# Optimization experiments

Measured on AMD Instinct MI355X. Metric: run time of the kernel, lower is better.

Reference implementation:

```python
import jax, jax.numpy as jnp
import numpy as np

N_P, N_V, N_C, N_A = 8000, 3000, 1500, 6000
CLS = N_C
D = 128
E = 150000
N_TOT = N_P + N_V + N_C + N_A
LAMBDA1 = 1.0


def _cal_matrix(A):
    # row-normalize, leaving all-zero rows untouched (matches cal_matrix)
    d = jnp.sum(A, axis=1)
    safe = jnp.where(d > 0, d, 1.0)
    return jnp.where((d > 0)[:, None], A / safe[:, None], A)


def _linear(x, W, b):
    return x @ W.T + b


def _gru(x, h, Wih, Whh, bih, bhh):
    # torch.nn.GRUCell semantics; gate order r, z, n
    gi = x @ Wih.T + bih
    gh = h @ Whh.T + bhh
    ir, iz, inn = jnp.split(gi, 3, axis=1)
    hr, hz, hn = jnp.split(gh, 3, axis=1)
    r = jax.nn.sigmoid(ir + hr)
    z = jax.nn.sigmoid(iz + hz)
    n = jnp.tanh(inn + r * hn)
    return (1.0 - z) * n + z * h


def _ce_soft(pred, label):
    # torch CrossEntropyLoss with probabilistic targets; NOTE: pred is already
    # softmaxed in the original, so log_softmax is applied on top (faithful double softmax)
    return -jnp.mean(jnp.sum(label * jax.nn.log_softmax(pred, axis=1), axis=1))


def _fuse(e0, e1, W2, b2, W3, b3):
    # attention fusion: leaky_relu(., 0) == relu; softmax over the NODE axis (faithful)
    a = jnp.concatenate([_linear(e0, W2, b2), _linear(e1, W3, b3)], axis=0)  # [2N,1]
    alpha = jax.nn.softmax(jax.nn.relu(a).reshape(2, -1, 1), axis=1)
    return jax.nn.relu(jnp.sum(alpha * jnp.stack([e0, e1], axis=0), axis=0))


def _forward(feat_P, feat_V, feat_C, feat_A, W1, b1, W2, b2, W3, b3,
             L00W, L00b, L01W, L01b, L10W, L10b, L11W, L11b, L12W, L12b,
             g0_Wih, g0_Whh, g0_bih, g0_bhh, g1_Wih, g1_Whh, g1_bih, g1_bhh,
             rel_emb, adj00, adj01, adj10, adj11, adj12, clsA, clsP, clsV, u_s, u_d):
    # self embeddings via shared linear1
    self_P = _linear(feat_P, W1, b1)
    self_V = _linear(feat_V, W1, b1)
    self_C = _linear(feat_C, W1, b1)
    self_A = _linear(feat_A, W1, b1)
    loss_tcp = jnp.float32(0.0)
    # ---- meta-path 0: V -> P -> A (GRUCell 0) ----
    pred = jax.nn.softmax(_linear(feat_V, L00W, L00b), axis=1)        # [N_V, CLS]
    loss_tcp += _ce_soft(pred, clsV)
    tcp = jnp.sum(pred * clsV, axis=1, keepdims=True)                 # bmm([N,1,C],[N,C,1])
    h = adj00 @ (tcp * feat_V)                                        # [N_P, D]
    state_P0 = _gru(feat_P, h, g0_Wih, g0_Whh, g0_bih, g0_bhh)
    pred = jax.nn.softmax(_linear(state_P0, L01W, L01b), axis=1)
    loss_tcp += _ce_soft(pred, clsP)
    tcp = jnp.sum(pred * clsP, axis=1, keepdims=True)
    h = adj01 @ (tcp * state_P0)                                      # [N_A, D]
    state_A0 = _gru(feat_A, h, g0_Wih, g0_Whh, g0_bih, g0_bhh)
    # ---- meta-path 1: A -> P -> V -> C (GRUCell 1) ----
    pred = jax.nn.softmax(_linear(feat_A, L10W, L10b), axis=1)
    loss_tcp += _ce_soft(pred, clsA)
    tcp = jnp.sum(pred * clsA, axis=1, keepdims=True)
    h = adj10 @ (tcp * feat_A)                                        # [N_P, D]
    state_P1 = _gru(feat_P, h, g1_Wih, g1_Whh, g1_bih, g1_bhh)        # appended 3rd, unused by fusion
    pred = jax.nn.softmax(_linear(state_P1, L11W, L11b), axis=1)
    loss_tcp += _ce_soft(pred, clsP)
    tcp = jnp.sum(pred * clsP, axis=1, keepdims=True)
    h = adj11 @ (tcp * state_P1)                                      # [N_V, D]
    state_V1 = _gru(feat_V, h, g1_Wih, g1_Whh, g1_bih, g1_bhh)
    pred = jax.nn.softmax(_linear(state_V1, L12W, L12b), axis=1)
    loss_tcp += _ce_soft(pred, clsV)
    tcp = jnp.sum(pred * clsV, axis=1, keepdims=True)
    h = adj12 @ (tcp * state_V1)                                      # [N_C, D]
    state_C1 = _gru(feat_C, h, g1_Wih, g1_Whh, g1_bih, g1_bhh)
    # ---- attention fusion of (self_emb, first GRU state) per node type ----
    emb_P = _fuse(self_P, state_P0, W2, b2, W3, b3)
    emb_V = _fuse(self_V, state_V1, W2, b2, W3, b3)
    emb_C = _fuse(self_C, state_C1, W2, b2, W3, b3)
    emb_A = _fuse(self_A, state_A0, W2, b2, W3, b3)
    final_ent = jnp.concatenate([emb_P, emb_V, emb_C, emb_A], axis=0)  # order P,V,C,A
    # ---- link scoring ----
    lab_d = u_d[:, 2].astype(jnp.float32)
    lab_s = u_s[:, 2].astype(jnp.float32)
    M_r = rel_emb[u_d[:, 3]]
    inner_d = jnp.sum(M_r * jnp.tanh(final_ent[u_d[:, 0]] + final_ent[u_d[:, 1]]), axis=1)
    inner_s = jnp.sum(final_ent[u_s[:, 0]] * final_ent[u_s[:, 1]], axis=1)
    base = -jnp.sum(jax.nn.log_sigmoid(lab_d * inner_d)) - jnp.sum(jax.nn.log_sigmoid(lab_s * inner_s))
    # l2_loss_emb is 0 in the original; l2_loss is computed but never added to loss_emb
    loss = base + LAMBDA1 * loss_tcp
    return loss, final_ent, rel_emb


def setup_inputs():
    key = jax.random.key(0)
    ki = iter(jax.random.split(key, 48))
    def nk():
        return next(ki)
    def xav(o, i):  # xavier_normal_
        return jax.random.normal(nk(), (o, i), jnp.float32) * jnp.sqrt(2.0 / (o + i))
    def uni(shape):  # torch GRUCell default init
        k = 1.0 / float(np.sqrt(D))
        return jax.random.uniform(nk(), shape, jnp.float32, -k, k)
    def radj(o, i, p=0.003):  # raw binary adjacency
        return (jax.random.uniform(nk(), (o, i)) < p).astype(jnp.float32)

    feat_P = jax.random.normal(nk(), (N_P, D), jnp.float32)
    feat_V = jax.random.normal(nk(), (N_V, D), jnp.float32)
    feat_C = jax.random.normal(nk(), (N_C, D), jnp.float32)
    feat_A = jax.random.normal(nk(), (N_A, D), jnp.float32)
    A00 = radj(N_P, N_V); A01 = radj(N_A, N_P)
    A10 = radj(N_P, N_A); A11 = radj(N_V, N_P); A12 = radj(N_C, N_V)

    inp = dict(
        feat_P=feat_P, feat_V=feat_V, feat_C=feat_C, feat_A=feat_A,
        W1=xav(D, D), b1=jnp.zeros((D,), jnp.float32),
        W2=xav(1, D), b2=jnp.zeros((1,), jnp.float32),
        W3=xav(1, D), b3=jnp.zeros((1,), jnp.float32),
        L00W=xav(CLS, D), L00b=jnp.zeros((CLS,), jnp.float32),
        L01W=xav(CLS, D), L01b=jnp.zeros((CLS,), jnp.float32),
        L10W=xav(CLS, D), L10b=jnp.zeros((CLS,), jnp.float32),
        L11W=xav(CLS, D), L11b=jnp.zeros((CLS,), jnp.float32),
        L12W=xav(CLS, D), L12b=jnp.zeros((CLS,), jnp.float32),
        g0_Wih=uni((3 * D, D)), g0_Whh=uni((3 * D, D)), g0_bih=uni((3 * D,)), g0_bhh=uni((3 * D,)),
        g1_Wih=uni((3 * D, D)), g1_Whh=uni((3 * D, D)), g1_bih=uni((3 * D,)), g1_bhh=uni((3 * D,)),
        rel_emb=jax.random.normal(nk(), (12, D), jnp.float32),
        adj00=_cal_matrix(A00), adj01=_cal_matrix(A01),
        adj10=_cal_matrix(A10), adj11=_cal_matrix(A11), adj12=_cal_matrix(A12),
        clsA=_cal_matrix((A12 @ (A11 @ A10)).T),   # [N_A, CLS]
        clsP=_cal_matrix((A12 @ A11).T),           # [N_P, CLS]
        clsV=_cal_matrix(A12.T),                   # [N_V, CLS]
    )

    def edges(n_cols):
        i = jax.random.randint(nk(), (E,), 0, N_TOT)
        j = jax.random.randint(nk(), (E,), 0, N_TOT)
        lab = jax.random.randint(nk(), (E,), 0, 2) * 2 - 1  # labels in {-1,+1}
        cols = [i, j, lab]
        if n_cols == 4:
            cols.append(jax.random.randint(nk(), (E,), 0, 12))
        return jnp.stack(cols, axis=1)

    inp['u_s'] = edges(3)
    inp['u_d'] = edges(4)
    return inp


def reference(feat_P, feat_V, feat_C, feat_A, W1, b1, W2, b2, W3, b3,
              L00W, L00b, L01W, L01b, L10W, L10b, L11W, L11b, L12W, L12b,
              g0_Wih, g0_Whh, g0_bih, g0_bhh, g1_Wih, g1_Whh, g1_bih, g1_bhh,
              rel_emb, adj00, adj01, adj10, adj11, adj12, clsA, clsP, clsV, u_s, u_d):
    return _forward(feat_P, feat_V, feat_C, feat_A, W1, b1, W2, b2, W3, b3,
                    L00W, L00b, L01W, L01b, L10W, L10b, L11W, L11b, L12W, L12b,
                    g0_Wih, g0_Whh, g0_bih, g0_bhh, g1_Wih, g1_Whh, g1_bih, g1_bhh,
                    rel_emb, adj00, adj01, adj10, adj11, adj12, clsA, clsP, clsV, u_s, u_d)
```

## Files before the change

### kernel.cpp

```cpp
#include <hip/hip_runtime.h>
#include <cstdint>
#include <cstddef>

#define DEV_INLINE __device__ __forceinline__

typedef __attribute__((ext_vector_type(8))) short bf16x8;
typedef __attribute__((ext_vector_type(16))) float f32x16;
struct __align__(8) US4 { unsigned short u[4]; };

DEV_INLINE unsigned short f2bf(float x) {
  unsigned u = __float_as_uint(x);
  return (unsigned short)((u + 0x7FFFu + ((u >> 16) & 1u)) >> 16);
}
DEV_INLINE float2 bfpair(unsigned v) {
  return make_float2(__uint_as_float(v << 16), __uint_as_float(v & 0xFFFF0000u));
}

struct CvtSeg { const float* src; unsigned short* dst; int n; int nblk; };
struct CvtArgs { CvtSeg seg[16]; int nseg; };

__global__ __launch_bounds__(256) void convert_bf16_many(CvtArgs args) {
  int b = blockIdx.x;
  int s = 0;
  while (s < args.nseg && b >= args.seg[s].nblk) { b -= args.seg[s].nblk; ++s; }
// ... 51 lines not shown
    acc1 = __builtin_amdgcn_mfma_f32_32x32x16_bf16(a, b1, acc1, 0, 0, 0);
  }

#pragma unroll
  for (int reg = 0; reg < 16; ++reg) {
    int r = bm + wave * 32 + (reg & 3) + 8 * (reg >> 2) + 4 * lhi;
    if (r < N) {
      int c0 = bn + l31;
      if (c0 < O) C[(size_t)r * O + c0] = acc0[reg] + bias[c0];
      int c1 = bn + 32 + l31;
      if (c1 < O) C[(size_t)r * O + c1] = acc1[reg] + bias[c1];
    }
  }
}

__global__ __launch_bounds__(256) void gemm_bf16(
    const unsigned short* __restrict__ Xb, const unsigned short* __restrict__ Wb,
    const float* __restrict__ bias, float* __restrict__ C, int N, int O)
{
  __shared__ __align__(16) unsigned short Xs[128 * 128];
  __shared__ __align__(16) unsigned short Ws[64 * 128];
  gemm_body(Xb, Wb, bias, C, N, O, blockIdx.x * 128, blockIdx.y * 64, Xs, Ws);
}

struct GSeg { const unsigned short* X; const unsigned short* W; const float* bias;
              float* C; int N; int O; int blk0; int xblk; };
struct GSegs { GSeg s[8]; int nseg; };

__global__ __launch_bounds__(256) void gemm_bf16_gseg(GSegs gs) {
  __shared__ __align__(16) unsigned short Xs[128 * 128];
  __shared__ __align__(16) unsigned short Ws[64 * 128];
  int bx = blockIdx.x;
  int si = 0;
  while (si + 1 < gs.nseg && bx >= gs.s[si + 1].blk0) ++si;
  const GSeg& g = gs.s[si];
  int b = bx - g.blk0;
  int bm = (b % g.xblk) * 128;
  int bn = (b / g.xblk) * 64;
  gemm_body(g.X, g.W, g.bias, g.C, g.N, g.O, bm, bn, Xs, Ws);
}

DEV_INLINE void ghgru_body(
    const unsigned short* __restrict__ Hb, const unsigned short* __restrict__ Whhb,
    const float* __restrict__ bhh, const float* __restrict__ gi,
    const float* __restrict__ hv, float* __restrict__ out,
    unsigned short* __restrict__ outb, int M, int bm, unsigned short* As)
{
  const int tid = threadIdx.x;
#pragma unroll
  for (int i = 0; i < 2; ++i) {
    int s = tid + 256 * i;
    int row = s >> 4, c16 = s & 15;
    uint4 v = make_uint4(0, 0, 0, 0);
    int gr = bm + row;
    if (gr < M) v = *reinterpret_cast<const uint4*>(Hb + (size_t)gr * 128 + c16 * 8);
    *reinterpret_cast<uint4*>(&As[(row * 16 + (c16 ^ (row & 7))) * 8]) = v;
  }
  __syncthreads();

  const int wave = tid >> 6, lane = tid & 63;
  const int l31 = lane & 31, lhi = lane >> 5;
  const int d = wave * 32 + l31;

  f32x16 ar, az, an;
#pragma unroll
  for (int i = 0; i < 16; ++i) { ar[i] = 0.f; az[i] = 0.f; an[i] = 0.f; }

#pragma unroll
  for (int ks = 0; ks < 8; ++ks) {
    int c16 = ks * 2 + lhi;
    bf16x8 a = *reinterpret_cast<const bf16x8*>(&As[(l31 * 16 + (c16 ^ (l31 & 7))) * 8]);
    const unsigned short* wb = Whhb + (size_t)c16 * 8;
    bf16x8 br = *reinterpret_cast<const bf16x8*>(wb + (size_t)d * 128);
    bf16x8 bz = *reinterpret_cast<const bf16x8*>(wb + (size_t)(128 + d) * 128);
    bf16x8 bn = *reinterpret_cast<const bf16x8*>(wb + (size_t)(256 + d) * 128);
    ar = __builtin_amdgcn_mfma_f32_32x32x16_bf16(a, br, ar, 0, 0, 0);
    az = __builtin_amdgcn_mfma_f32_32x32x16_bf16(a, bz, az, 0, 0, 0);
    an = __builtin_amdgcn_mfma_f32_32x32x16_bf16(a, bn, an, 0, 0, 0);
  }

  const float b_r = bhh[d], b_z = bhh[128 + d], b_n = bhh[256 + d];
#pragma unroll
  for (int reg = 0; reg < 16; ++reg) {
    int r = bm + (reg & 3) + 8 * (reg >> 2) + 4 * lhi;
    if (r < M) {
      const float* gir = gi + (size_t)r * 384;
      float rr = 1.f / (1.f + expf(-(gir[d] + ar[reg] + b_r)));
      float zz = 1.f / (1.f + expf(-(gir[128 + d] + az[reg] + b_z)));
      float nn = tanhf(gir[256 + d] + rr * (an[reg] + b_n));
      float h = hv[(size_t)r * 128 + d];
      float o = (1.f - zz) * nn + zz * h;
      out[(size_t)r * 128 + d] = o;
      outb[(size_t)r * 128 + d] = f2bf(o);
    }
  }
}

__global__ __launch_bounds__(256) void gh_gru(
    const unsigned short* __restrict__ Hb, const unsigned short* __restrict__ Whhb,
    const float* __restrict__ bhh, const float* __restrict__ gi,
    const float* __restrict__ hv, float* __restrict__ out,
    unsigned short* __restrict__ outb, int M)
{
  __shared__ __align__(16) unsigned short As[32 * 128];
  ghgru_body(Hb, Whhb, bhh, gi, hv, out, outb, M, blockIdx.x * 32, As);
}

__global__ __launch_bounds__(256) void gh_gru2(
    const unsigned short* Hb0, const unsigned short* Whh0, const float* bhh0,
    const float* gi0, const float* hv0, float* out0, unsigned short* outb0,
    int M0, int nblk0,
    const unsigned short* Hb1, const unsigned short* Whh1, const float* bhh1,
    const float* gi1, const float* hv1, float* out1, unsigned short* outb1, int M1)
{
  __shared__ __align__(16) unsigned short As[32 * 128];
  if ((int)blockIdx.x < nblk0)
    ghgru_body(Hb0, Whh0, bhh0, gi0, hv0, out0, outb0, M0, blockIdx.x * 32, As);
  else
    ghgru_body(Hb1, Whh1, bhh1, gi1, hv1, out1, outb1, M1, (blockIdx.x - nblk0) * 32, As);
}

DEV_INLINE void spmv_body(const float* __restrict__ A, const float* __restrict__ Xs,
                          float* __restrict__ H, unsigned short* __restrict__ Hb,
                          int row, int K, float (*red)[128])
{
  int tid = threadIdx.x, wave = tid >> 6, lane = tid & 63;
  const float4* Arow = reinterpret_cast<const float4*>(A + (size_t)row * K);
  int K4 = K >> 2;
  float acc0 = 0.f, acc1 = 0.f;
  for (int base = wave * 64; base < K4; base += 256) {
    int q = base + lane;
    float4 a = (q < K4) ? Arow[q] : make_float4(0.f, 0.f, 0.f, 0.f);
#pragma unroll
    for (int c = 0; c < 4; ++c) {
      float av = (c == 0) ? a.x : (c == 1) ? a.y : (c == 2) ? a.z : a.w;
      unsigned long long mm = __ballot(av != 0.f);
      while (mm) {
        int b = __builtin_ctzll(mm);
        mm &= mm - 1;
        float v = __shfl(av, b);
        int jj = (base + b) * 4 + c;
        const float* xr = Xs + (size_t)jj * 128;
        acc0 += v * xr[lane];
        acc1 += v * xr[lane + 64];
      }
    }
  }
  red[wave][lane] = acc0;
  red[wave][lane + 64] = acc1;
  __syncthreads();
  if (wave == 0) {
    float r0 = red[0][lane] + red[1][lane] + red[2][lane] + red[3][lane];
    float r1 = red[0][lane + 64] + red[1][lane + 64] + red[2][lane + 64] + red[3][lane + 64];
    H[(size_t)row * 128 + lane] = r0;
    H[(size_t)row * 128 + 64 + lane] = r1;
    Hb[(size_t)row * 128 + lane] = f2bf(r0);
    Hb[(size_t)row * 128 + 64 + lane] = f2bf(r1);
  }
}

__global__ __launch_bounds__(256) void spmv_scan(
    const float* __restrict__ A, const float* __restrict__ Xs,
    float* __restrict__ H, unsigned short* __restrict__ Hb, int M, int K)
{
  __shared__ float red[4][128];
  spmv_body(A, Xs, H, Hb, blockIdx.x, K, red);
}

__global__ __launch_bounds__(256) void spmv_scan2(
    const float* __restrict__ A0, const float* __restrict__ X0,
    float* __restrict__ H0, unsigned short* __restrict__ H0b, int M0, int K0,
    const float* __restrict__ A1, const float* __restrict__ X1,
    float* __restrict__ H1, unsigned short* __restrict__ H1b, int K1)
{
  __shared__ float red[4][128];
  if ((int)blockIdx.x < M0) spmv_body(A0, X0, H0, H0b, blockIdx.x, K0, red);
  else                      spmv_body(A1, X1, H1, H1b, blockIdx.x - M0, K1, red);
}

DEV_INLINE void rowops_body(int lane, const float4* __restrict__ lr,
                            const float4* __restrict__ cr,
                            const float* __restrict__ srcrow,
                            float* __restrict__ scaledrow, float* __restrict__ cep)
{
  float4 e[6];
  float m = -3.4e38f;
#pragma unroll
  for (int k = 0; k < 6; ++k) {
    int idx = k * 64 + lane;
    if (idx < 375) {
      e[k] = lr[idx];
      m = fmaxf(m, fmaxf(fmaxf(e[k].x, e[k].y), fmaxf(e[k].z, e[k].w)));
    } else {
      e[k] = make_float4(-3.4e38f, -3.4e38f, -3.4e38f, -3.4e38f);
    }
  }
#pragma unroll
  for (int o = 1; o < 64; o <<= 1) m = fmaxf(m, __shfl_xor(m, o));
  float z = 0.f;
#pragma unroll
  for (int k = 0; k < 6; ++k) {
    e[k].x = expf(e[k].x - m); e[k].y = expf(e[k].y - m);
    e[k].z = expf(e[k].z - m); e[k].w = expf(e[k].w - m);
    z += (e[k].x + e[k].y) + (e[k].z + e[k].w);
  }
#pragma unroll
  for (int o = 1; o < 64; o <<= 1) z += __shfl_xor(z, o);
  float invZ1 = 1.0f / z;
  float m2 = invZ1;
  float t = 0.f, ls = 0.f, z2 = 0.f;
#pragma unroll
  for (int k = 0; k < 6; ++k) {
    int idx = k * 64 + lane;
    if (idx < 375) {
      float4 c = cr[idx];
      float px = e[k].x * invZ1, py = e[k].y * invZ1;
      float pz = e[k].z * invZ1, pw = e[k].w * invZ1;
      t  += c.x * px + c.y * py + c.z * pz + c.w * pw;
      ls += (c.x + c.y) + (c.z + c.w);
      z2 += expf(px - m2) + expf(py - m2) + expf(pz - m2) + expf(pw - m2);
    }
  }
#pragma unroll
  for (int o = 1; o < 64; o <<= 1) {
    t += __shfl_xor(t, o); ls += __shfl_xor(ls, o); z2 += __shfl_xor(z2, o);
  }
  if (lane == 0) *cep = t - ls * (m2 + logf(z2));
  scaledrow[lane]      = t * srcrow[lane];
  scaledrow[lane + 64] = t * srcrow[lane + 64];
}

__global__ __launch_bounds__(256) void rowops_wave(
    const float* __restrict__ logits, const float* __restrict__ cls,
    const float* __restrict__ src, float* __restrict__ scaled,
    float* __restrict__ ce, int N)
{
  int gw = (blockIdx.x * 256 + threadIdx.x) >> 6;
  if (gw >= N) return;
  int lane = threadIdx.x & 63;
  rowops_body(lane,
              reinterpret_cast<const float4*>(logits + (size_t)gw * 1500),
              reinterpret_cast<const float4*>(cls + (size_t)gw * 1500),
              src + (size_t)gw * 128, scaled + (size_t)gw * 128, ce + gw);
}

__global__ __launch_bounds__(256) void rowops2(
    const float* lgA, const float* clsA_, const float* srcA, float* scA, float* ceA, int nA,
    const float* lgB, const float* clsB_, const float* srcB, float* scB, float* ceB, int nB)
{
  int gw = (blockIdx.x * 256 + threadIdx.x) >> 6;
  if (gw >= nA + nB) return;
  int lane = threadIdx.x & 63;
  if (gw < nA) {
    rowops_body(lane,
                reinterpret_cast<const float4*>(lgA + (size_t)gw * 1500),
                reinterpret_cast<const float4*>(clsA_ + (size_t)gw * 1500),
                srcA + (size_t)gw * 128, scA + (size_t)gw * 128, ceA + gw);
  } else {
    int r = gw - nA;
    rowops_body(lane,
                reinterpret_cast<const float4*>(lgB + (size_t)r * 1500),
                reinterpret_cast<const float4*>(clsB_ + (size_t)r * 1500),
                srcB + (size_t)r * 128, scB + (size_t)r * 128, ceB + r);
  }
}

__global__ __launch_bounds__(256) void fuse_scores_all(
    const float* __restrict__ e0, const float* __restrict__ e1,
    const float* __restrict__ W2, const float* __restrict__ b2,
    const float* __restrict__ W3, const float* __restrict__ b3,
    float* __restrict__ s0, float* __restrict__ s1)
{
  int lane = threadIdx.x & 63;
  int row = (blockIdx.x * 256 + threadIdx.x) >> 6;
  if (row >= 18500) return;
  float a0 = e0[(size_t)row * 128 + lane] * W2[lane] + e0[(size_t)row * 128 + 64 + lane] * W2[64 + lane];
  float a1 = e1[(size_t)row * 128 + lane] * W3[lane] + e1[(size_t)row * 128 + 64 + lane] * W3[64 + lane];
#pragma unroll
  for (int o = 32; o > 0; o >>= 1) { a0 += __shfl_down(a0, o); a1 += __shfl_down(a1, o); }
// ... 9 lines not shown
{
  __shared__ float red[1024];
  const int ns[4]   = {8000, 3000, 1500, 6000};
  const int offs[4] = {0, 8000, 11000, 12500};
  int b = blockIdx.x;
  int n = ns[b];
  const float* p0 = s0 + offs[b];
  const float* p1 = s1 + offs[b];
  int tid = threadIdx.x;
  float m = -3.4e38f;
  for (int i = tid; i < n; i += 1024) m = fmaxf(m, p0[i]);
  red[tid] = m; __syncthreads();
  for (int s = 512; s > 0; s >>= 1) { if (tid < s) red[tid] = fmaxf(red[tid], red[tid + s]); __syncthreads(); }
  float m0 = red[0]; __syncthreads();
  float z = 0.f;
  for (int i = tid; i < n; i += 1024) z += expf(p0[i] - m0);
  red[tid] = z; __syncthreads();
  for (int s = 512; s > 0; s >>= 1) { if (tid < s) red[tid] += red[tid + s]; __syncthreads(); }
  float Z0 = red[0]; __syncthreads();
  m = -3.4e38f;
  for (int i = tid; i < n; i += 1024) m = fmaxf(m, p1[i]);
  red[tid] = m; __syncthreads();
  for (int s = 512; s > 0; s >>= 1) { if (tid < s) red[tid] = fmaxf(red[tid], red[tid + s]); __syncthreads(); }
  float m1 = red[0]; __syncthreads();
  z = 0.f;
  for (int i = tid; i < n; i += 1024) z += expf(p1[i] - m1);
  red[tid] = z; __syncthreads();
  for (int s = 512; s > 0; s >>= 1) { if (tid < s) red[tid] += red[tid + s]; __syncthreads(); }
  if (tid == 0) { den[b * 4] = m0; den[b * 4 + 1] = Z0; den[b * 4 + 2] = m1; den[b * 4 + 3] = red[0]; }
}

__global__ __launch_bounds__(256) void fuse_emb_all(
    const float* __restrict__ e0, const float* __restrict__ e1,
    const float* __restrict__ s0, const float* __restrict__ s1,
    const float* __restrict__ den, const float* __restrict__ rel,
    float* __restrict__ fe, unsigned short* __restrict__ feb,
    float* __restrict__ rel_out)
{
  int t = blockIdx.x * 256 + threadIdx.x;
  const int tot2 = 18500 * 64;
  if (t < tot2) {
    int idx = t * 2;
    int row = idx >> 7;
    int e = (row < 8000) ? 0 : (row < 11000) ? 1 : (row < 12500) ? 2 : 3;
    float a0 = expf(s0[row] - den[e * 4]) / den[e * 4 + 1];
    float a1 = expf(s1[row] - den[e * 4 + 2]) / den[e * 4 + 3];
    float2 v0 = *reinterpret_cast<const float2*>(e0 + idx);
    float2 v1 = *reinterpret_cast<const float2*>(e1 + idx);
    float r0 = fmaxf(a0 * v0.x + a1 * v1.x, 0.f);
    float r1 = fmaxf(a0 * v0.y + a1 * v1.y, 0.f);
    *reinterpret_cast<float2*>(fe + idx) = make_float2(r0, r1);
    unsigned pb = (unsigned)f2bf(r0) | ((unsigned)f2bf(r1) << 16);
    *reinterpret_cast<unsigned*>(feb + idx) = pb;
  } else if (t < tot2 + 768) {
    int k = (t - tot2) * 2;
    *reinterpret_cast<float2*>(rel_out + k) = *reinterpret_cast<const float2*>(rel + k);
  }
}

__global__ __launch_bounds__(256) void edge_both(
    const int* __restrict__ ud, const int* __restrict__ us,
// ... 6 lines not shown
  int bb = is_d ? blockIdx.x : blockIdx.x - 1024;
  int gw = bb * 4 + wid;
  const int nw = 1024 * 4;
  float acc = 0.f;
  if (is_d) {
    for (int e = gw; e < En; e += nw) {
      int4 ei = *reinterpret_cast<const int4*>(ud + (size_t)e * 4);
      float2 fi = bfpair(reinterpret_cast<const unsigned*>(feb + (size_t)ei.x * 128)[lane]);
      float2 fj = bfpair(reinterpret_cast<const unsigned*>(feb + (size_t)ei.y * 128)[lane]);
      float2 rr = bfpair(reinterpret_cast<const unsigned*>(relb + (size_t)ei.w * 128)[lane]);
      float d = rr.x * tanhf(fi.x + fj.x) + rr.y * tanhf(fi.y + fj.y);
#pragma unroll
      for (int o = 32; o > 0; o >>= 1) d += __shfl_down(d, o);
      if (lane == 0) {
        float x = (float)ei.z * d;
        acc += (x >= 0.f) ? log1pf(expf(-x)) : (-x + log1pf(expf(x)));
      }
    }
  } else {
    for (int e = gw; e < En; e += nw) {
      int i = us[(size_t)e * 3], j = us[(size_t)e * 3 + 1], lab = us[(size_t)e * 3 + 2];
      float2 fi = bfpair(reinterpret_cast<const unsigned*>(feb + (size_t)i * 128)[lane]);
      float2 fj = bfpair(reinterpret_cast<const unsigned*>(feb + (size_t)j * 128)[lane]);
      float d = fi.x * fj.x + fi.y * fj.y;
#pragma unroll
      for (int o = 32; o > 0; o >>= 1) d += __shfl_down(d, o);
      if (lane == 0) {
        float x = (float)lab * d;
        acc += (x >= 0.f) ? log1pf(expf(-x)) : (-x + log1pf(expf(x)));
      }
    }
  }
  __shared__ float red[4];
  if (lane == 0) red[wid] = acc;
  __syncthreads();
  if (threadIdx.x == 0) partial[blockIdx.x] = red[0] + red[1] + red[2] + red[3];
}

__global__ __launch_bounds__(1024) void final_reduce(
    const float* __restrict__ partial, const float* __restrict__ cebuf,
    float* __restrict__ out)
{
  __shared__ float red[1024];
  __shared__ float total;
// ... 62 lines not shown
  const float* clsV = (const float*)d_in[36];
  const int* u_s = (const int*)d_in[37];
  const int* u_d = (const int*)d_in[38];

  float* out = (float*)d_out;
  float* fe = out + 1;
  float* rel_out = out + 1 + 18500 * 128;

  float* ws = (float*)d_ws;
  size_t o = 0;
  auto alloc = [&](size_t n) { float* p = ws + o; o += n; return p; };
  float* selfb   = alloc((size_t)18500 * 128);
  float* stcat   = alloc((size_t)18500 * 128);
  float* stP1    = alloc((size_t)8000 * 128);
  float* gi      = alloc((size_t)26500 * 384);
  float* logits  = alloc((size_t)8000 * 1500);
  float* logits0 = alloc((size_t)3000 * 1500);
  float* logits2 = alloc((size_t)8000 * 1500);
  float* scaled1 = alloc((size_t)8000 * 128);
  float* scaled3 = alloc((size_t)8000 * 128);
  float* scaled0 = alloc((size_t)3000 * 128);
  float* scaled2 = alloc((size_t)6000 * 128);
  float* scaled4 = alloc((size_t)3000 * 128);
  float* h0      = alloc((size_t)8000 * 128);
  float* h2      = alloc((size_t)8000 * 128);
  float* h1      = alloc((size_t)6000 * 128);
  float* h3      = alloc((size_t)3000 * 128);
  float* h4      = alloc((size_t)1500 * 128);
  float* cebuf   = alloc(5 * 8000);
  float* s0b = alloc(18500);
  float* s1b = alloc(18500);
  float* den = alloc(16);
  float* partial = alloc(2048);
  auto allocb = [&](size_t nelem) { unsigned short* p = (unsigned short*)(ws + o); o += (nelem + 1) / 2; return p; };
  unsigned short* featb  = allocb((size_t)18500 * 128);
  unsigned short* stcatb = allocb((size_t)18500 * 128);
  unsigned short* stP1b  = allocb((size_t)8000 * 128);
  unsigned short* feb    = allocb((size_t)18500 * 128);
  unsigned short* h0b    = allocb((size_t)8000 * 128);
  unsigned short* h2b    = allocb((size_t)8000 * 128);
  unsigned short* h1b    = allocb((size_t)6000 * 128);
  unsigned short* h3b    = allocb((size_t)3000 * 128);
  unsigned short* h4b    = allocb((size_t)1500 * 128);
  unsigned short* relb   = allocb(12 * 128);
  unsigned short* W1b = allocb(128 * 128);
  unsigned short* L00Wb = allocb(1500 * 128);
  unsigned short* L01Wb = allocb(1500 * 128);
  unsigned short* L10Wb = allocb(1500 * 128);
  unsigned short* L11Wb = allocb(1500 * 128);
  unsigned short* L12Wb = allocb(1500 * 128);
  unsigned short* g0Wihb = allocb(384 * 128);
  unsigned short* g0Whhb = allocb(384 * 128);
  unsigned short* g1Wihb = allocb(384 * 128);
  unsigned short* g1Whhb = allocb(384 * 128);
  unsigned short* featPb = featb;
  unsigned short* featVb = featb + (size_t)8000 * 128;
  unsigned short* featCb = featb + (size_t)11000 * 128;
  unsigned short* featAb = featb + (size_t)12500 * 128;
// ... 32 lines not shown
  addseg(rel_emb, relb, 12 * 128);
  ca.nseg = nseg;
  hipLaunchKernelGGL(convert_bf16_many, dim3(totblk), blk, 0, stream, ca);

  const size_t giOff[5] = {0, 8000, 14000, 22000, 25000};

  {
    GSegs gs{};
    int nb = 0, k = 0;
    auto add = [&](const unsigned short* X, const unsigned short* W, const float* bias,
                   float* C, int N, int O) {
      int xb = (N + 127) / 128, yb = (O + 63) / 64;
      gs.s[k] = GSeg{X, W, bias, C, N, O, nb, xb};
      nb += xb * yb; ++k;
    };
    add(featb,  W1b,    b1,     selfb,             18500, 128);
    add(featPb, g0Wihb, g0_bih, gi + giOff[0] * 384, 8000, 384);
    add(featAb, g0Wihb, g0_bih, gi + giOff[1] * 384, 6000, 384);
    add(featPb, g1Wihb, g1_bih, gi + giOff[2] * 384, 8000, 384);
    add(featVb, g1Wihb, g1_bih, gi + giOff[3] * 384, 3000, 384);
    add(featCb, g1Wihb, g1_bih, gi + giOff[4] * 384, 1500, 384);
    add(featVb, L00Wb,  L00b,   logits0,            3000, 1500);
    add(featAb, L10Wb,  L10b,   logits2,            6000, 1500);
    gs.nseg = k;
    hipLaunchKernelGGL(gemm_bf16_gseg, dim3(nb), blk, 0, stream, gs);
  }

  hipLaunchKernelGGL(rowops2, dim3((9000 * 64 + 255) / 256), blk, 0, stream,
                     logits0, clsV, feat_V, scaled0, cebuf + 0 * 8000, 3000,
                     logits2, clsA, feat_A, scaled2, cebuf + 2 * 8000, 6000);
  hipLaunchKernelGGL(spmv_scan2, dim3(16000), blk, 0, stream,
                     adj00, scaled0, h0, h0b, 8000, 3000,
                     adj10, scaled2, h2, h2b, 6000);
  hipLaunchKernelGGL(gh_gru2, dim3(500), blk, 0, stream,
                     h0b, g0Whhb, g0_bhh, gi + giOff[0] * 384, h0, stP0, stP0b, 8000, 250,
                     h2b, g1Whhb, g1_bhh, gi + giOff[2] * 384, h2, stP1, stP1b, 8000);
  {
    GSegs gs{};
    gs.s[0] = GSeg{stP0b, L01Wb, L01b, logits,  8000, 1500, 0,    63};
    gs.s[1] = GSeg{stP1b, L11Wb, L11b, logits2, 8000, 1500, 1512, 63};
    gs.nseg = 2;
    hipLaunchKernelGGL(gemm_bf16_gseg, dim3(3024), blk, 0, stream, gs);
  }
  hipLaunchKernelGGL(rowops2, dim3((16000 * 64 + 255) / 256), blk, 0, stream,
                     logits,  clsP, stP0, scaled1, cebuf + 1 * 8000, 8000,
                     logits2, clsP, stP1, scaled3, cebuf + 3 * 8000, 8000);
  hipLaunchKernelGGL(spmv_scan2, dim3(9000), blk, 0, stream,
                     adj01, scaled1, h1, h1b, 6000, 8000,
                     adj11, scaled3, h3, h3b, 8000);
  hipLaunchKernelGGL(gh_gru2, dim3(188 + 94), blk, 0, stream,
                     h1b, g0Whhb, g0_bhh, gi + giOff[1] * 384, h1, stA0, stA0b, 6000, 188,
                     h3b, g1Whhb, g1_bhh, gi + giOff[3] * 384, h3, stV1, stV1b, 3000);
  hipLaunchKernelGGL(gemm_bf16, dim3(24, 24), blk, 0, stream, stV1b, L12Wb, L12b, logits, 3000, 1500);
  hipLaunchKernelGGL(rowops_wave, dim3((3000 * 64 + 255) / 256), blk, 0, stream,
                     logits, clsV, stV1, scaled4, cebuf + 4 * 8000, 3000);
  hipLaunchKernelGGL(spmv_scan, dim3(1500), blk, 0, stream, adj12, scaled4, h4, h4b, 1500, 3000);
  hipLaunchKernelGGL(gh_gru, dim3(47), blk, 0, stream,
                     h4b, g1Whhb, g1_bhh, gi + giOff[4] * 384, h4, stC1, stC1b, 1500);

  hipLaunchKernelGGL(fuse_scores_all, dim3((18500 + 3) / 4), blk, 0, stream,
                     selfb, stcat, W2, b2, W3, b3, s0b, s1b);
  hipLaunchKernelGGL(denom4, dim3(4), dim3(1024), 0, stream, s0b, s1b, den);
  hipLaunchKernelGGL(fuse_emb_all, dim3((18500 * 64 + 768 + 255) / 256), blk, 0, stream,
                     selfb, stcat, s0b, s1b, den, rel_emb, fe, feb, rel_out);

  hipLaunchKernelGGL(edge_both, dim3(2048), blk, 0, stream, u_d, u_s, feb, relb, partial, 150000);

  hipLaunchKernelGGL(final_reduce, dim3(1), dim3(1024), 0, stream, partial, cebuf, out);
}
```

Before: 555.4 us.

## Fuse logits GEMM with softmax-CE rowops and SpMV with GRU

Replaces the separate large logits GEMMs and row-wise softmax/cross-entropy kernels with one kernel per stage. Each block computes 32 rows of logits with MFMA twice, once for the softmax denominator and once for the CE and tcp terms, so the logit matrices are never written to or read back from memory. The adjacency SpMV is merged into the GRU kernel: each block builds its 32 h rows in LDS and feeds them straight into the Whh MFMAs, removing the h and h-bf16 intermediate buffers. Several expf calls become __expf. In exchange, the first softmax no longer subtracts the row max, which can overflow for large logits. SpMV parallelism also drops from four waves per row to one wave handling eight rows in sequence.

```diff
diff --git a/kernel.cpp b/kernel.cpp
--- a/kernel.cpp
+++ b/kernel.cpp
@@ -89,15 +89,6 @@
   }
 }
 
-__global__ __launch_bounds__(256) void gemm_bf16(
-    const unsigned short* __restrict__ Xb, const unsigned short* __restrict__ Wb,
-    const float* __restrict__ bias, float* __restrict__ C, int N, int O)
-{
-  __shared__ __align__(16) unsigned short Xs[128 * 128];
-  __shared__ __align__(16) unsigned short Ws[64 * 128];
-  gemm_body(Xb, Wb, bias, C, N, O, blockIdx.x * 128, blockIdx.y * 64, Xs, Ws);
-}
-
 struct GSeg { const unsigned short* X; const unsigned short* W; const float* bias;
               float* C; int N; int O; int blk0; int xblk; };
 struct GSegs { GSeg s[8]; int nseg; };
@@ -115,11 +106,13 @@
   gemm_body(g.X, g.W, g.bias, g.C, g.N, g.O, bm, bn, Xs, Ws);
 }
 
-DEV_INLINE void ghgru_body(
-    const unsigned short* __restrict__ Hb, const unsigned short* __restrict__ Whhb,
-    const float* __restrict__ bhh, const float* __restrict__ gi,
-    const float* __restrict__ hv, float* __restrict__ out,
-    unsigned short* __restrict__ outb, int M, int bm, unsigned short* As)
+struct LRSeg { const unsigned short* X; const unsigned short* W; const float* bias;
+               const float* cls; const float* src; float* scaled; float* ce;
+               int N; int blk0; };
+
+DEV_INLINE void lrops_body(const LRSeg& g, int bm,
+    unsigned short* As, float* Zrow, float* Trow,
+    float (*redA)[32], float (*redB)[32], float (*redC)[32])
 {
   const int tid = threadIdx.x;
 #pragma unroll
@@ -128,13 +121,178 @@
     int row = s >> 4, c16 = s & 15;
     uint4 v = make_uint4(0, 0, 0, 0);
     int gr = bm + row;
-    if (gr < M) v = *reinterpret_cast<const uint4*>(Hb + (size_t)gr * 128 + c16 * 8);
+    if (gr < g.N) v = *reinterpret_cast<const uint4*>(g.X + (size_t)gr * 128 + c16 * 8);
     *reinterpret_cast<uint4*>(&As[(row * 16 + (c16 ^ (row & 7))) * 8]) = v;
   }
   __syncthreads();
 
   const int wave = tid >> 6, lane = tid & 63;
   const int l31 = lane & 31, lhi = lane >> 5;
+
+  bf16x8 af[8];
+#pragma unroll
+  for (int ks = 0; ks < 8; ++ks)
+    af[ks] = *reinterpret_cast<const bf16x8*>(&As[(l31 * 16 + ((ks * 2 + lhi) ^ (l31 & 7)) ) * 8]);
+
+  float zp[16];
+#pragma unroll
+  for (int i = 0; i < 16; ++i) zp[i] = 0.f;
+  for (int t = wave; t < 47; t += 4) {
+    int col = t * 32 + l31;
+    bool valid = col < 1500;
+    int colc = valid ? col : 1499;
+    float bc = g.bias[colc];
+    f32x16 acc;
+#pragma unroll
+    for (int i = 0; i < 16; ++i) acc[i] = 0.f;
+#pragma unroll
+    for (int ks = 0; ks < 8; ++ks) {
+      bf16x8 b = *reinterpret_cast<const bf16x8*>(g.W + (size_t)colc * 128 + (ks * 2 + lhi) * 8);
+      acc = __builtin_amdgcn_mfma_f32_32x32x16_bf16(af[ks], b, acc, 0, 0, 0);
+    }
+#pragma unroll
+    for (int r = 0; r < 16; ++r)
+      zp[r] += valid ? __expf(acc[r] + bc) : 0.f;
+  }
+#pragma unroll
+  for (int o = 1; o < 32; o <<= 1)
+#pragma unroll
+    for (int r = 0; r < 16; ++r) zp[r] += __shfl_xor(zp[r], o);
+  if (l31 == 0) {
+#pragma unroll
+    for (int r = 0; r < 16; ++r)
+      redA[wave][(r & 3) + 8 * (r >> 2) + 4 * lhi] = zp[r];
+  }
+  __syncthreads();
+  if (tid < 32) Zrow[tid] = redA[0][tid] + redA[1][tid] + redA[2][tid] + redA[3][tid];
+  __syncthreads();
+
+  float invZ[16];
+#pragma unroll
+  for (int r = 0; r < 16; ++r) invZ[r] = 1.f / Zrow[(r & 3) + 8 * (r >> 2) + 4 * lhi];
+
+  float tp[16], lp[16], qp[16];
+#pragma unroll
+  for (int i = 0; i < 16; ++i) { tp[i] = 0.f; lp[i] = 0.f; qp[i] = 0.f; }
+  for (int t = wave; t < 47; t += 4) {
+    int col = t * 32 + l31;
+    bool valid = col < 1500;
+    int colc = valid ? col : 1499;
+    float bc = g.bias[colc];
+    f32x16 acc;
+#pragma unroll
+    for (int i = 0; i < 16; ++i) acc[i] = 0.f;
+#pragma unroll
+    for (int ks = 0; ks < 8; ++ks) {
+      bf16x8 b = *reinterpret_cast<const bf16x8*>(g.W + (size_t)colc * 128 + (ks * 2 + lhi) * 8);
+      acc = __builtin_amdgcn_mfma_f32_32x32x16_bf16(af[ks], b, acc, 0, 0, 0);
+    }
+#pragma unroll
+    for (int r = 0; r < 16; ++r) {
+      int rowl = (r & 3) + 8 * (r >> 2) + 4 * lhi;
+      int grow = bm + rowl;
+      float c = (valid && grow < g.N) ? g.cls[(size_t)grow * 1500 + col] : 0.f;
+      float e = valid ? __expf(acc[r] + bc) : 0.f;
+      float p = e * invZ[r];
+      tp[r] += c * p;
+      lp[r] += c;
+      qp[r] += valid ? __expf(p) : 0.f;
+    }
+  }
+#pragma unroll
+  for (int o = 1; o < 32; o <<= 1)
+#pragma unroll
+    for (int r = 0; r < 16; ++r) {
+      tp[r] += __shfl_xor(tp[r], o);
+      lp[r] += __shfl_xor(lp[r], o);
+      qp[r] += __shfl_xor(qp[r], o);
+    }
+  if (l31 == 0) {
+#pragma unroll
+    for (int r = 0; r < 16; ++r) {
+      int rowl = (r & 3) + 8 * (r >> 2) + 4 * lhi;
+      redA[wave][rowl] = tp[r];
+      redB[wave][rowl] = lp[r];
+      redC[wave][rowl] = qp[r];
+    }
+  }
+  __syncthreads();
+  if (tid < 32) {
+    float T = redA[0][tid] + redA[1][tid] + redA[2][tid] + redA[3][tid];
+    float L = redB[0][tid] + redB[1][tid] + redB[2][tid] + redB[3][tid];
+    float Q = redC[0][tid] + redC[1][tid] + redC[2][tid] + redC[3][tid];
+    Trow[tid] = T;
+    int grow = bm + tid;
+    if (grow < g.N) g.ce[grow] = T - L * logf(Q);
+  }
+  __syncthreads();
+  for (int i = tid; i < 32 * 128; i += 256) {
+    int r = i >> 7, d = i & 127;
+    int grow = bm + r;
+    if (grow < g.N) g.scaled[(size_t)grow * 128 + d] = Trow[r] * g.src[(size_t)grow * 128 + d];
+  }
+}
+
+__global__ __launch_bounds__(256) void logits_rowops1(LRSeg s0) {
+  __shared__ __align__(16) unsigned short As[32 * 128];
+  __shared__ float Zrow[32], Trow[32];
+  __shared__ float redA[4][32], redB[4][32], redC[4][32];
+  lrops_body(s0, blockIdx.x * 32, As, Zrow, Trow, redA, redB, redC);
+}
+
+__global__ __launch_bounds__(256) void logits_rowops2(LRSeg s0, LRSeg s1) {
+  __shared__ __align__(16) unsigned short As[32 * 128];
+  __shared__ float Zrow[32], Trow[32];
+  __shared__ float redA[4][32], redB[4][32], redC[4][32];
+  if ((int)blockIdx.x < s1.blk0)
+    lrops_body(s0, blockIdx.x * 32, As, Zrow, Trow, redA, redB, redC);
+  else
+    lrops_body(s1, (blockIdx.x - s1.blk0) * 32, As, Zrow, Trow, redA, redB, redC);
+}
+
+struct SGSeg { const float* A; const float* Xs; const unsigned short* Whh;
+               const float* bhh; const float* gi; float* out;
+               unsigned short* outb; int M; int K; int blk0; };
+
+DEV_INLINE void spmvgru_body(const SGSeg& g, int bm, float* Hs, unsigned short* Hsb)
+{
+  const int tid = threadIdx.x;
+  const int wave = tid >> 6, lane = tid & 63;
+  const int K4 = g.K >> 2;
+  for (int rr = 0; rr < 8; ++rr) {
+    int rowl = wave * 8 + rr;
+    int grow = bm + rowl;
+    float acc0 = 0.f, acc1 = 0.f;
+    if (grow < g.M) {
+      const float4* Arow = reinterpret_cast<const float4*>(g.A + (size_t)grow * g.K);
+      for (int base = 0; base < K4; base += 64) {
+        int q = base + lane;
+        float4 a = (q < K4) ? Arow[q] : make_float4(0.f, 0.f, 0.f, 0.f);
+#pragma unroll
+        for (int c = 0; c < 4; ++c) {
+          float av = (c == 0) ? a.x : (c == 1) ? a.y : (c == 2) ? a.z : a.w;
+          unsigned long long mm = __ballot(av != 0.f);
+          while (mm) {
+            int b = __builtin_ctzll(mm);
+            mm &= mm - 1;
+            float v = __shfl(av, b);
+            int jj = (base + b) * 4 + c;
+            const float* xr = g.Xs + (size_t)jj * 128;
+            acc0 += v * xr[lane];
+            acc1 += v * xr[lane + 64];
+          }
+        }
+      }
+    }
+    Hs[rowl * 128 + lane] = acc0;
+    Hs[rowl * 128 + 64 + lane] = acc1;
+    int d0 = lane, d1 = lane + 64;
+    Hsb[(rowl * 16 + ((d0 >> 3) ^ (rowl & 7))) * 8 + (d0 & 7)] = f2bf(acc0);
+    Hsb[(rowl * 16 + ((d1 >> 3) ^ (rowl & 7))) * 8 + (d1 & 7)] = f2bf(acc1);
+  }
+  __syncthreads();
+
+  const int l31 = lane & 31, lhi = lane >> 5;
   const int d = wave * 32 + l31;
 
   f32x16 ar, az, an;
@@ -144,8 +302,8 @@
 #pragma unroll
   for (int ks = 0; ks < 8; ++ks) {
     int c16 = ks * 2 + lhi;
-    bf16x8 a = *reinterpret_cast<const bf16x8*>(&As[(l31 * 16 + (c16 ^ (l31 & 7))) * 8]);
-    const unsigned short* wb = Whhb + (size_t)c16 * 8;
+    bf16x8 a = *reinterpret_cast<const bf16x8*>(&Hsb[(l31 * 16 + (c16 ^ (l31 & 7))) * 8]);
+    const unsigned short* wb = g.Whh + (size_t)c16 * 8;
     bf16x8 br = *reinterpret_cast<const bf16x8*>(wb + (size_t)d * 128);
     bf16x8 bz = *reinterpret_cast<const bf16x8*>(wb + (size_t)(128 + d) * 128);
     bf16x8 bn = *reinterpret_cast<const bf16x8*>(wb + (size_t)(256 + d) * 128);
@@ -154,190 +312,37 @@
     an = __builtin_amdgcn_mfma_f32_32x32x16_bf16(a, bn, an, 0, 0, 0);
   }
 
-  const float b_r = bhh[d], b_z = bhh[128 + d], b_n = bhh[256 + d];
+  const float b_r = g.bhh[d], b_z = g.bhh[128 + d], b_n = g.bhh[256 + d];
 #pragma unroll
   for (int reg = 0; reg < 16; ++reg) {
-    int r = bm + (reg & 3) + 8 * (reg >> 2) + 4 * lhi;
-    if (r < M) {
-      const float* gir = gi + (size_t)r * 384;
-      float rr = 1.f / (1.f + expf(-(gir[d] + ar[reg] + b_r)));
-      float zz = 1.f / (1.f + expf(-(gir[128 + d] + az[reg] + b_z)));
+    int rowl = (reg & 3) + 8 * (reg >> 2) + 4 * lhi;
+    int grow = bm + rowl;
+    if (grow < g.M) {
+      const float* gir = g.gi + (size_t)grow * 384;
+      float rr = 1.f / (1.f + __expf(-(gir[d] + ar[reg] + b_r)));
+      float zz = 1.f / (1.f + __expf(-(gir[128 + d] + az[reg] + b_z)));
       float nn = tanhf(gir[256 + d] + rr * (an[reg] + b_n));
-      float h = hv[(size_t)r * 128 + d];
+      float h = Hs[rowl * 128 + d];
       float o = (1.f - zz) * nn + zz * h;
-      out[(size_t)r * 128 + d] = o;
-      outb[(size_t)r * 128 + d] = f2bf(o);
-    }
-  }
-}
-
-__global__ __launch_bounds__(256) void gh_gru(
-    const unsigned short* __restrict__ Hb, const unsigned short* __restrict__ Whhb,
-    const float* __restrict__ bhh, const float* __restrict__ gi,
-    const float* __restrict__ hv, float* __restrict__ out,
-    unsigned short* __restrict__ outb, int M)
-{
-  __shared__ __align__(16) unsigned short As[32 * 128];
-  ghgru_body(Hb, Whhb, bhh, gi, hv, out, outb, M, blockIdx.x * 32, As);
-}
-
-__global__ __launch_bounds__(256) void gh_gru2(
-    const unsigned short* Hb0, const unsigned short* Whh0, const float* bhh0,
-    const float* gi0, const float* hv0, float* out0, unsigned short* outb0,
-    int M0, int nblk0,
-    const unsigned short* Hb1, const unsigned short* Whh1, const float* bhh1,
-    const float* gi1, const float* hv1, float* out1, unsigned short* outb1, int M1)
-{
-  __shared__ __align__(16) unsigned short As[32 * 128];
-  if ((int)blockIdx.x < nblk0)
-    ghgru_body(Hb0, Whh0, bhh0, gi0, hv0, out0, outb0, M0, blockIdx.x * 32, As);
+      g.out[(size_t)grow * 128 + d] = o;
+      g.outb[(size_t)grow * 128 + d] = f2bf(o);
+    }
+  }
+}
+
+__global__ __launch_bounds__(256) void spmv_gru1(SGSeg s0) {
+  __shared__ float Hs[32 * 128];
+  __shared__ __align__(16) unsigned short Hsb[32 * 128];
+  spmvgru_body(s0, blockIdx.x * 32, Hs, Hsb);
+}
+
+__global__ __launch_bounds__(256) void spmv_gru2(SGSeg s0, SGSeg s1) {
+  __shared__ float Hs[32 * 128];
+  __shared__ __align__(16) unsigned short Hsb[32 * 128];
+  if ((int)blockIdx.x < s1.blk0)
+    spmvgru_body(s0, blockIdx.x * 32, Hs, Hsb);
   else
-    ghgru_body(Hb1, Whh1, bhh1, gi1, hv1, out1, outb1, M1, (blockIdx.x - nblk0) * 32, As);
-}
-
-DEV_INLINE void spmv_body(const float* __restrict__ A, const float* __restrict__ Xs,
-                          float* __restrict__ H, unsigned short* __restrict__ Hb,
-                          int row, int K, float (*red)[128])
-{
-  int tid = threadIdx.x, wave = tid >> 6, lane = tid & 63;
-  const float4* Arow = reinterpret_cast<const float4*>(A + (size_t)row * K);
-  int K4 = K >> 2;
-  float acc0 = 0.f, acc1 = 0.f;
-  for (int base = wave * 64; base < K4; base += 256) {
-    int q = base + lane;
-    float4 a = (q < K4) ? Arow[q] : make_float4(0.f, 0.f, 0.f, 0.f);
-#pragma unroll
-    for (int c = 0; c < 4; ++c) {
-      float av = (c == 0) ? a.x : (c == 1) ? a.y : (c == 2) ? a.z : a.w;
-      unsigned long long mm = __ballot(av != 0.f);
-      while (mm) {
-        int b = __builtin_ctzll(mm);
-        mm &= mm - 1;
-        float v = __shfl(av, b);
-        int jj = (base + b) * 4 + c;
-        const float* xr = Xs + (size_t)jj * 128;
-        acc0 += v * xr[lane];
-        acc1 += v * xr[lane + 64];
-      }
-    }
-  }
-  red[wave][lane] = acc0;
-  red[wave][lane + 64] = acc1;
-  __syncthreads();
-  if (wave == 0) {
-    float r0 = red[0][lane] + red[1][lane] + red[2][lane] + red[3][lane];
-    float r1 = red[0][lane + 64] + red[1][lane + 64] + red[2][lane + 64] + red[3][lane + 64];
-    H[(size_t)row * 128 + lane] = r0;
-    H[(size_t)row * 128 + 64 + lane] = r1;
-    Hb[(size_t)row * 128 + lane] = f2bf(r0);
-    Hb[(size_t)row * 128 + 64 + lane] = f2bf(r1);
-  }
-}
-
-__global__ __launch_bounds__(256) void spmv_scan(
-    const float* __restrict__ A, const float* __restrict__ Xs,
-    float* __restrict__ H, unsigned short* __restrict__ Hb, int M, int K)
-{
-  __shared__ float red[4][128];
-  spmv_body(A, Xs, H, Hb, blockIdx.x, K, red);
-}
-
-__global__ __launch_bounds__(256) void spmv_scan2(
-    const float* __restrict__ A0, const float* __restrict__ X0,
-    float* __restrict__ H0, unsigned short* __restrict__ H0b, int M0, int K0,
-    const float* __restrict__ A1, const float* __restrict__ X1,
-    float* __restrict__ H1, unsigned short* __restrict__ H1b, int K1)
-{
-  __shared__ float red[4][128];
-  if ((int)blockIdx.x < M0) spmv_body(A0, X0, H0, H0b, blockIdx.x, K0, red);
-  else                      spmv_body(A1, X1, H1, H1b, blockIdx.x - M0, K1, red);
-}
-
-DEV_INLINE void rowops_body(int lane, const float4* __restrict__ lr,
-                            const float4* __restrict__ cr,
-                            const float* __restrict__ srcrow,
-                            float* __restrict__ scaledrow, float* __restrict__ cep)
-{
-  float4 e[6];
-  float m = -3.4e38f;
-#pragma unroll
-  for (int k = 0; k < 6; ++k) {
-    int idx = k * 64 + lane;
-    if (idx < 375) {
-      e[k] = lr[idx];
-      m = fmaxf(m, fmaxf(fmaxf(e[k].x, e[k].y), fmaxf(e[k].z, e[k].w)));
-    } else {
-      e[k] = make_float4(-3.4e38f, -3.4e38f, -3.4e38f, -3.4e38f);
-    }
-  }
-#pragma unroll
-  for (int o = 1; o < 64; o <<= 1) m = fmaxf(m, __shfl_xor(m, o));
-  float z = 0.f;
-#pragma unroll
-  for (int k = 0; k < 6; ++k) {
-    e[k].x = expf(e[k].x - m); e[k].y = expf(e[k].y - m);
-    e[k].z = expf(e[k].z - m); e[k].w = expf(e[k].w - m);
-    z += (e[k].x + e[k].y) + (e[k].z + e[k].w);
-  }
-#pragma unroll
-  for (int o = 1; o < 64; o <<= 1) z += __shfl_xor(z, o);
-  float invZ1 = 1.0f / z;
-  float m2 = invZ1;
-  float t = 0.f, ls = 0.f, z2 = 0.f;
-#pragma unroll
-  for (int k = 0; k < 6; ++k) {
-    int idx = k * 64 + lane;
-    if (idx < 375) {
-      float4 c = cr[idx];
-      float px = e[k].x * invZ1, py = e[k].y * invZ1;
-      float pz = e[k].z * invZ1, pw = e[k].w * invZ1;
-      t  += c.x * px + c.y * py + c.z * pz + c.w * pw;
-      ls += (c.x + c.y) + (c.z + c.w);
-      z2 += expf(px - m2) + expf(py - m2) + expf(pz - m2) + expf(pw - m2);
-    }
-  }
-#pragma unroll
-  for (int o = 1; o < 64; o <<= 1) {
-    t += __shfl_xor(t, o); ls += __shfl_xor(ls, o); z2 += __shfl_xor(z2, o);
-  }
-  if (lane == 0) *cep = t - ls * (m2 + logf(z2));
-  scaledrow[lane]      = t * srcrow[lane];
-  scaledrow[lane + 64] = t * srcrow[lane + 64];
-}
-
-__global__ __launch_bounds__(256) void rowops_wave(
-    const float* __restrict__ logits, const float* __restrict__ cls,
-    const float* __restrict__ src, float* __restrict__ scaled,
-    float* __restrict__ ce, int N)
-{
-  int gw = (blockIdx.x * 256 + threadIdx.x) >> 6;
-  if (gw >= N) return;
-  int lane = threadIdx.x & 63;
-  rowops_body(lane,
-              reinterpret_cast<const float4*>(logits + (size_t)gw * 1500),
-              reinterpret_cast<const float4*>(cls + (size_t)gw * 1500),
-              src + (size_t)gw * 128, scaled + (size_t)gw * 128, ce + gw);
-}
-
-__global__ __launch_bounds__(256) void rowops2(
-    const float* lgA, const float* clsA_, const float* srcA, float* scA, float* ceA, int nA,
-    const float* lgB, const float* clsB_, const float* srcB, float* scB, float* ceB, int nB)
-{
-  int gw = (blockIdx.x * 256 + threadIdx.x) >> 6;
-  if (gw >= nA + nB) return;
-  int lane = threadIdx.x & 63;
-  if (gw < nA) {
-    rowops_body(lane,
-                reinterpret_cast<const float4*>(lgA + (size_t)gw * 1500),
-                reinterpret_cast<const float4*>(clsA_ + (size_t)gw * 1500),
-                srcA + (size_t)gw * 128, scA + (size_t)gw * 128, ceA + gw);
-  } else {
-    int r = gw - nA;
-    rowops_body(lane,
-                reinterpret_cast<const float4*>(lgB + (size_t)r * 1500),
-                reinterpret_cast<const float4*>(clsB_ + (size_t)r * 1500),
-                srcB + (size_t)r * 128, scB + (size_t)r * 128, ceB + r);
-  }
+    spmvgru_body(s1, (blockIdx.x - s1.blk0) * 32, Hs, Hsb);
 }
 
 __global__ __launch_bounds__(256) void fuse_scores_all(
@@ -377,7 +382,7 @@
   for (int s = 512; s > 0; s >>= 1) { if (tid < s) red[tid] = fmaxf(red[tid], red[tid + s]); __syncthreads(); }
   float m0 = red[0]; __syncthreads();
   float z = 0.f;
-  for (int i = tid; i < n; i += 1024) z += expf(p0[i] - m0);
+  for (int i = tid; i < n; i += 1024) z += __expf(p0[i] - m0);
   red[tid] = z; __syncthreads();
   for (int s = 512; s > 0; s >>= 1) { if (tid < s) red[tid] += red[tid + s]; __syncthreads(); }
   float Z0 = red[0]; __syncthreads();
@@ -387,7 +392,7 @@
   for (int s = 512; s > 0; s >>= 1) { if (tid < s) red[tid] = fmaxf(red[tid], red[tid + s]); __syncthreads(); }
   float m1 = red[0]; __syncthreads();
   z = 0.f;
-  for (int i = tid; i < n; i += 1024) z += expf(p1[i] - m1);
+  for (int i = tid; i < n; i += 1024) z += __expf(p1[i] - m1);
   red[tid] = z; __syncthreads();
   for (int s = 512; s > 0; s >>= 1) { if (tid < s) red[tid] += red[tid + s]; __syncthreads(); }
   if (tid == 0) { den[b * 4] = m0; den[b * 4 + 1] = Z0; den[b * 4 + 2] = m1; den[b * 4 + 3] = red[0]; }
@@ -406,8 +411,8 @@
     int idx = t * 2;
     int row = idx >> 7;
     int e = (row < 8000) ? 0 : (row < 11000) ? 1 : (row < 12500) ? 2 : 3;
-    float a0 = expf(s0[row] - den[e * 4]) / den[e * 4 + 1];
-    float a1 = expf(s1[row] - den[e * 4 + 2]) / den[e * 4 + 3];
+    float a0 = __expf(s0[row] - den[e * 4]) / den[e * 4 + 1];
+    float a1 = __expf(s1[row] - den[e * 4 + 2]) / den[e * 4 + 3];
     float2 v0 = *reinterpret_cast<const float2*>(e0 + idx);
     float2 v1 = *reinterpret_cast<const float2*>(e1 + idx);
     float r0 = fmaxf(a0 * v0.x + a1 * v1.x, 0.f);
@@ -444,7 +449,7 @@
       for (int o = 32; o > 0; o >>= 1) d += __shfl_down(d, o);
       if (lane == 0) {
         float x = (float)ei.z * d;
-        acc += (x >= 0.f) ? log1pf(expf(-x)) : (-x + log1pf(expf(x)));
+        acc += (x >= 0.f) ? log1pf(__expf(-x)) : (-x + log1pf(__expf(x)));
       }
     }
   } else {
@@ -457,7 +462,7 @@
       for (int o = 32; o > 0; o >>= 1) d += __shfl_down(d, o);
       if (lane == 0) {
         float x = (float)lab * d;
-        acc += (x >= 0.f) ? log1pf(expf(-x)) : (-x + log1pf(expf(x)));
+        acc += (x >= 0.f) ? log1pf(__expf(-x)) : (-x + log1pf(__expf(x)));
       }
     }
   }
@@ -550,19 +555,11 @@
   float* stcat   = alloc((size_t)18500 * 128);
   float* stP1    = alloc((size_t)8000 * 128);
   float* gi      = alloc((size_t)26500 * 384);
-  float* logits  = alloc((size_t)8000 * 1500);
-  float* logits0 = alloc((size_t)3000 * 1500);
-  float* logits2 = alloc((size_t)8000 * 1500);
+  float* scaled0 = alloc((size_t)3000 * 128);
   float* scaled1 = alloc((size_t)8000 * 128);
+  float* scaled2 = alloc((size_t)6000 * 128);
   float* scaled3 = alloc((size_t)8000 * 128);
-  float* scaled0 = alloc((size_t)3000 * 128);
-  float* scaled2 = alloc((size_t)6000 * 128);
   float* scaled4 = alloc((size_t)3000 * 128);
-  float* h0      = alloc((size_t)8000 * 128);
-  float* h2      = alloc((size_t)8000 * 128);
-  float* h1      = alloc((size_t)6000 * 128);
-  float* h3      = alloc((size_t)3000 * 128);
-  float* h4      = alloc((size_t)1500 * 128);
   float* cebuf   = alloc(5 * 8000);
   float* s0b = alloc(18500);
   float* s1b = alloc(18500);
@@ -573,11 +570,6 @@
   unsigned short* stcatb = allocb((size_t)18500 * 128);
   unsigned short* stP1b  = allocb((size_t)8000 * 128);
   unsigned short* feb    = allocb((size_t)18500 * 128);
-  unsigned short* h0b    = allocb((size_t)8000 * 128);
-  unsigned short* h2b    = allocb((size_t)8000 * 128);
-  unsigned short* h1b    = allocb((size_t)6000 * 128);
-  unsigned short* h3b    = allocb((size_t)3000 * 128);
-  unsigned short* h4b    = allocb((size_t)1500 * 128);
   unsigned short* relb   = allocb(12 * 128);
   unsigned short* W1b = allocb(128 * 128);
   unsigned short* L00Wb = allocb(1500 * 128);
@@ -640,49 +632,44 @@
       gs.s[k] = GSeg{X, W, bias, C, N, O, nb, xb};
       nb += xb * yb; ++k;
     };
-    add(featb,  W1b,    b1,     selfb,             18500, 128);
+    add(featb,  W1b,    b1,     selfb,               18500, 128);
     add(featPb, g0Wihb, g0_bih, gi + giOff[0] * 384, 8000, 384);
     add(featAb, g0Wihb, g0_bih, gi + giOff[1] * 384, 6000, 384);
     add(featPb, g1Wihb, g1_bih, gi + giOff[2] * 384, 8000, 384);
     add(featVb, g1Wihb, g1_bih, gi + giOff[3] * 384, 3000, 384);
     add(featCb, g1Wihb, g1_bih, gi + giOff[4] * 384, 1500, 384);
-    add(featVb, L00Wb,  L00b,   logits0,            3000, 1500);
-    add(featAb, L10Wb,  L10b,   logits2,            6000, 1500);
     gs.nseg = k;
     hipLaunchKernelGGL(gemm_bf16_gseg, dim3(nb), blk, 0, stream, gs);
   }
 
-  hipLaunchKernelGGL(rowops2, dim3((9000 * 64 + 255) / 256), blk, 0, stream,
-                     logits0, clsV, feat_V, scaled0, cebuf + 0 * 8000, 3000,
-                     logits2, clsA, feat_A, scaled2, cebuf + 2 * 8000, 6000);
-  hipLaunchKernelGGL(spmv_scan2, dim3(16000), blk, 0, stream,
-                     adj00, scaled0, h0, h0b, 8000, 3000,
-                     adj10, scaled2, h2, h2b, 6000);
-  hipLaunchKernelGGL(gh_gru2, dim3(500), blk, 0, stream,
-                     h0b, g0Whhb, g0_bhh, gi + giOff[0] * 384, h0, stP0, stP0b, 8000, 250,
-                     h2b, g1Whhb, g1_bhh, gi + giOff[2] * 384, h2, stP1, stP1b, 8000);
   {
-    GSegs gs{};
-    gs.s[0] = GSeg{stP0b, L01Wb, L01b, logits,  8000, 1500, 0,    63};
-    gs.s[1] = GSeg{stP1b, L11Wb, L11b, logits2, 8000, 1500, 1512, 63};
-    gs.nseg = 2;
-    hipLaunchKernelGGL(gemm_bf16_gseg, dim3(3024), blk, 0, stream, gs);
-  }
-  hipLaunchKernelGGL(rowops2, dim3((16000 * 64 + 255) / 256), blk, 0, stream,
-                     logits,  clsP, stP0, scaled1, cebuf + 1 * 8000, 8000,
-                     logits2, clsP, stP1, scaled3, cebuf + 3 * 8000, 8000);
-  hipLaunchKernelGGL(spmv_scan2, dim3(9000), blk, 0, stream,
-                     adj01, scaled1, h1, h1b, 6000, 8000,
-                     adj11, scaled3, h3, h3b, 8000);
-  hipLaunchKernelGGL(gh_gru2, dim3(188 + 94), blk, 0, stream,
-                     h1b, g0Whhb, g0_bhh, gi + giOff[1] * 384, h1, stA0, stA0b, 6000, 188,
-                     h3b, g1Whhb, g1_bhh, gi + giOff[3] * 384, h3, stV1, stV1b, 3000);
-  hipLaunchKernelGGL(gemm_bf16, dim3(24, 24), blk, 0, stream, stV1b, L12Wb, L12b, logits, 3000, 1500);
-  hipLaunchKernelGGL(rowops_wave, dim3((3000 * 64 + 255) / 256), blk, 0, stream,
-                     logits, clsV, stV1, scaled4, cebuf + 4 * 8000, 3000);
-  hipLaunchKernelGGL(spmv_scan, dim3(1500), blk, 0, stream, adj12, scaled4, h4, h4b, 1500, 3000);
-  hipLaunchKernelGGL(gh_gru, dim3(47), blk, 0, stream,
-                     h4b, g1Whhb, g1_bhh, gi + giOff[4] * 384, h4, stC1, stC1b, 1500);
+    LRSeg a{featVb, L00Wb, L00b, clsV, feat_V, scaled0, cebuf + 0 * 8000, 3000, 0};
+    LRSeg b{featAb, L10Wb, L10b, clsA, feat_A, scaled2, cebuf + 2 * 8000, 6000, 94};
+    hipLaunchKernelGGL(logits_rowops2, dim3(94 + 188), blk, 0, stream, a, b);
+  }
+  {
+    SGSeg a{adj00, scaled0, g0Whhb, g0_bhh, gi + giOff[0] * 384, stP0, stP0b, 8000, 3000, 0};
+    SGSeg b{adj10, scaled2, g1Whhb, g1_bhh, gi + giOff[2] * 384, stP1, stP1b, 8000, 6000, 250};
+    hipLaunchKernelGGL(spmv_gru2, dim3(500), blk, 0, stream, a, b);
+  }
+  {
+    LRSeg a{stP0b, L01Wb, L01b, clsP, stP0, scaled1, cebuf + 1 * 8000, 8000, 0};
+    LRSeg b{stP1b, L11Wb, L11b, clsP, stP1, scaled3, cebuf + 3 * 8000, 8000, 250};
+    hipLaunchKernelGGL(logits_rowops2, dim3(500), blk, 0, stream, a, b);
+  }
+  {
+    SGSeg a{adj01, scaled1, g0Whhb, g0_bhh, gi + giOff[1] * 384, stA0, stA0b, 6000, 8000, 0};
+    SGSeg b{adj11, scaled3, g1Whhb, g1_bhh, gi + giOff[3] * 384, stV1, stV1b, 3000, 8000, 188};
+    hipLaunchKernelGGL(spmv_gru2, dim3(188 + 94), blk, 0, stream, a, b);
+  }
+  {
+    LRSeg a{stV1b, L12Wb, L12b, clsV, stV1, scaled4, cebuf + 4 * 8000, 3000, 0};
+    hipLaunchKernelGGL(logits_rowops1, dim3(94), blk, 0, stream, a);
+  }
+  {
+    SGSeg a{adj12, scaled4, g1Whhb, g1_bhh, gi + giOff[4] * 384, stC1, stC1b, 1500, 3000, 0};
+    hipLaunchKernelGGL(spmv_gru1, dim3(47), blk, 0, stream, a);
+  }
 
   hipLaunchKernelGGL(fuse_scores_all, dim3((18500 + 3) / 4), blk, 0, stream,
                      selfb, stcat, W2, b2, W3, b3, s0b, s1b);
```

Result: slower. 888.2 us (+59.9%).
